# Kernel tuning notes

Measured on AMD Instinct MI355X. Metric: run time of the kernel, lower is better.

## Reference

```python
import math
import jax, jax.numpy as jnp
import numpy as np

D_MODEL = 1024
N_HEADS = 16
D_K = D_MODEL // N_HEADS
B, T = 2, 2048


def setup_inputs() -> dict:
    key = jax.random.key(0)
    kx, kq, kk, kv, ko = jax.random.split(key, 5)
    x = jax.random.normal(kx, (B, T, D_MODEL), dtype=jnp.float32)
    # causal mask, 1 = keep, 0 = masked (broadcast over batch & heads)
    mask = jnp.tril(jnp.ones((T, T), dtype=jnp.int32))[None, None, :, :]
    s = 1.0 / math.sqrt(D_MODEL)
    # nn.Linear stores weight as [out, in]; y = x @ W.T
    W_q = jax.random.normal(kq, (D_MODEL, D_MODEL), dtype=jnp.float32) * s
    W_k = jax.random.normal(kk, (D_MODEL, D_MODEL), dtype=jnp.float32) * s
    W_v = jax.random.normal(kv, (D_MODEL, D_MODEL), dtype=jnp.float32) * s
    W_o = jax.random.normal(ko, (D_MODEL, D_MODEL), dtype=jnp.float32) * s
    return {"x": x, "mask": mask, "W_q": W_q, "W_k": W_k, "W_v": W_v, "W_o": W_o}


def _split_heads(y):
    # [B,T,D] -> [B,H,T,d_k]
    b, t, _ = y.shape
    return y.reshape(b, t, N_HEADS, D_K).transpose(0, 2, 1, 3)


def reference(x, mask, W_q, W_k, W_v, W_o):
    Q = _split_heads(x @ W_q.T)
    K = _split_heads(x @ W_k.T)
    V = _split_heads(x @ W_v.T)
    scores = jnp.einsum("bhqd,bhkd->bhqk", Q, K) / math.sqrt(D_K)
    scores = jnp.where(mask == 0, -jnp.inf, scores)
    attn = jax.nn.softmax(scores, axis=-1)
    out = jnp.einsum("bhqk,bhkd->bhqd", attn, V)
    out = out.transpose(0, 2, 1, 3).reshape(x.shape[0], x.shape[1], D_MODEL)
    return out @ W_o.T
```

## Files before the change

### kernel.cpp

```cpp
#include <hip/hip_runtime.h>

typedef __attribute__((ext_vector_type(8))) short short8;
typedef __attribute__((ext_vector_type(4))) float f32x4;
typedef __attribute__((ext_vector_type(16))) float f32x16;
typedef __attribute__((ext_vector_type(4))) unsigned short u16x4;
typedef __attribute__((ext_vector_type(4))) unsigned int u32x4;

#define T_SEQ   2048
#define NHEADS  16
#define DHEAD   64
#define DMODEL  1024
#define NBATCH  2
#define MROWS   (NBATCH * T_SEQ)

__device__ __forceinline__ unsigned short f2bf(float f) {
    unsigned int u = __float_as_uint(f);
    u += 0x7fffu + ((u >> 16) & 1u);
    return (unsigned short)(u >> 16);
}

__device__ __forceinline__ unsigned int cvtpk(float lo, float hi) {
    unsigned int r;
    asm("v_cvt_pk_bf16_f32 %0, %1, %2" : "=v"(r) : "v"(lo), "v"(hi));
    return r;
}

__device__ __forceinline__ void pl32(int a, int b, int& r0, int& r1) {
    auto r = __builtin_amdgcn_permlane32_swap(a, b, false, false);
    r0 = r[0]; r1 = r[1];
}

__device__ __forceinline__ void gld_lds16(const void* g, void* l) {
    __builtin_amdgcn_global_load_lds(
        (const __attribute__((address_space(1))) void*)g,
        (__attribute__((address_space(3))) void*)l, 16, 0, 0);
}

#define N8X (MROWS * DMODEL / 8)
#define N8W (DMODEL * DMODEL / 8)
__global__ __launch_bounds__(256) void k_convert_all(const float* __restrict__ x,
                                                     const float* __restrict__ w0,
                                                     const float* __restrict__ w1,
                                                     const float* __restrict__ w2,
                                                     const float* __restrict__ w3,
                                                     unsigned short* __restrict__ xbf,
                                                     unsigned short* __restrict__ wbf) {
    int i = blockIdx.x * blockDim.x + threadIdx.x;
    const float* src;
    unsigned short* dst;
    if (i < N8X) {
        src = x + (size_t)i * 8;
        dst = xbf + (size_t)i * 8;
    } else {
        int j = i - N8X;
        int which = j >> 17;
        const float* w = (which == 0) ? w0 : (which == 1) ? w1 : (which == 2) ? w2 : w3;
        src = w + (size_t)(j & (N8W - 1)) * 8;
        dst = wbf + (size_t)j * 8;
    }
    const float4* p = (const float4*)src;
    float4 a = p[0], b = p[1];
    short8 r;
    r[0] = (short)f2bf(a.x); r[1] = (short)f2bf(a.y);
    r[2] = (short)f2bf(a.z); r[3] = (short)f2bf(a.w);
    r[4] = (short)f2bf(b.x); r[5] = (short)f2bf(b.y);
    r[6] = (short)f2bf(b.z); r[7] = (short)f2bf(b.w);
    *(short8*)dst = r;
}

template <int MODE>
__global__ __launch_bounds__(256) void k_gemm_st(const unsigned short* __restrict__ A,
                                                 const unsigned short* __restrict__ Wm,
                                                 float* __restrict__ outF,
                                                 unsigned short* __restrict__ outQ,
                                                 unsigned short* __restrict__ outK,
                                                 unsigned short* __restrict__ outV) {
    __shared__ __align__(16) unsigned short smA[2][128 * 32];
    __shared__ __align__(16) unsigned short smB[2][128 * 32];
    const int tid  = threadIdx.x;
    const int lane = tid & 63;
    const int w    = tid >> 6;
    const int lr   = lane & 15;
    const int lg   = lane >> 4;
    const int flat = blockIdx.x;
    const int x8   = flat & 7;
    const int jj_  = flat >> 3;
    const int n0   = (x8 + 8 * (jj_ >> 5)) * 128;
    const int m0   = (jj_ & 31) * 128;
    const int wm   = (w >> 1) * 64;
    const int wn   = (w & 1) * 64;

    const int srow = w * 32 + (lane >> 2);
    const int scol = (((lane & 3) ^ ((lane >> 3) & 3))) * 8;
    const unsigned short* gA0 = A  + (size_t)(m0 + srow) * DMODEL + scol;
    const unsigned short* gB0 = Wm + (size_t)(n0 + srow) * DMODEL + scol;
    const int lo = w * 1024;
    const int sw = (lg ^ ((lr >> 1) & 3)) * 8;

    f32x4 acc[4][4];
#pragma unroll
    for (int i = 0; i < 4; i++)
#pragma unroll
        for (int j = 0; j < 4; j++) acc[i][j] = (f32x4){0.f, 0.f, 0.f, 0.f};

#define STAGE(K0, BUF) do {                                            \
        gld_lds16(gA0 + (K0),               smA[BUF] + lo);            \
        gld_lds16(gA0 + 16 * DMODEL + (K0), smA[BUF] + lo + 16 * 32);  \
        gld_lds16(gB0 + (K0),               smB[BUF] + lo);            \
        gld_lds16(gB0 + 16 * DMODEL + (K0), smB[BUF] + lo + 16 * 32);  \
    } while (0)

#define FRAG_READ(BUF)                                                           \
        short8 af[4], bfr[4];                                                    \
        {                                                                        \
            const unsigned short* sA = smA[BUF];                                 \
            const unsigned short* sB = smB[BUF];                                 \
            _Pragma("unroll")                                                    \
            for (int i = 0; i < 4; i++)                                          \
                af[i] = *(const short8*)&sA[(wm + 16 * i + lr) * 32 + sw];       \
            _Pragma("unroll")                                                    \
            for (int j = 0; j < 4; j++)                                          \
                bfr[j] = *(const short8*)&sB[(wn + 16 * j + lr) * 32 + sw];      \
        }

#define MFMA16()                                                                 \
        _Pragma("unroll")                                                        \
        for (int i = 0; i < 4; i++)                                              \
            _Pragma("unroll")                                                    \
            for (int j = 0; j < 4; j++)                                          \
                acc[i][j] = __builtin_amdgcn_mfma_f32_16x16x32_bf16(             \
                    af[i], bfr[j], acc[i][j], 0, 0, 0);

    STAGE(0, 0);
    STAGE(32, 1);

    for (int t = 0; t < 30; ++t) {
        asm volatile("s_waitcnt vmcnt(4)" ::: "memory");
        __builtin_amdgcn_s_barrier();
        FRAG_READ(t & 1)
        asm volatile("s_waitcnt lgkmcnt(0)" ::: "memory");
        __builtin_amdgcn_sched_barrier(0);
        __builtin_amdgcn_s_barrier();
        STAGE((t + 2) * 32, t & 1);
        MFMA16()
    }
    {
        asm volatile("s_waitcnt vmcnt(4)" ::: "memory");
        __builtin_amdgcn_s_barrier();
        FRAG_READ(0)
        MFMA16()
    }
    {
        asm volatile("s_waitcnt vmcnt(0)" ::: "memory");
        __builtin_amdgcn_s_barrier();
        FRAG_READ(1)
        MFMA16()
    }
#undef STAGE
#undef FRAG_READ
#undef MFMA16

    if (MODE == 0) {
#pragma unroll
        for (int i = 0; i < 4; i++)
#pragma unroll
            for (int j = 0; j < 4; j++) {
                int n = n0 + wn + 16 * j + lr;
#pragma unroll
                for (int r = 0; r < 4; r++) {
                    int mm = m0 + wm + 16 * i + lg * 4 + r;
                    outF[(size_t)mm * DMODEL + n] = acc[i][j][r];
                }
            }
    } else {
        const int which = n0 >> 10;
        const int nb = n0 & 1023;
        const float QS = 0.18033688f;
#pragma unroll
        for (int i = 0; i < 4; i++)
#pragma unroll
            for (int j = 0; j < 4; j++) {
                int nloc = nb + wn + 16 * j + lr;
                int h = nloc >> 6, d = nloc & 63;
                int mb = m0 + wm + 16 * i + lg * 4;
                int b = mb >> 11, t = mb & (T_SEQ - 1);
                size_t base = (size_t)(b * NHEADS + h) * T_SEQ * DHEAD;
                if (which == 2) {
                    int off = ((((t >> 6) * 2 + (d >> 5)) * 4 + ((t >> 4) & 3)) * 64
                               + ((t >> 3) & 1) * 32 + (d & 31)) * 8 + (t & 7);
                    u16x4 pk;
#pragma unroll
                    for (int r = 0; r < 4; r++) pk[r] = f2bf(acc[i][j][r]);
                    *(u16x4*)(outV + base + off) = pk;
                } else {
                    unsigned short* dst = (which == 0) ? outQ : outK;
                    const float sc = (which == 0) ? QS : 1.0f;
                    int off = (((t >> 5) * 4 + (d >> 4)) * 64 + (d & 8) * 4 + (t & 31)) * 8 + (d & 7);
#pragma unroll
                    for (int r = 0; r < 4; r++)
                        dst[base + off + r * 8] = f2bf(acc[i][j][r] * sc);
                }
            }
    }
}

__global__ __launch_bounds__(256) void k_gemm_o(const unsigned short* __restrict__ A,
                                                const unsigned short* __restrict__ Wm,
                                                float* __restrict__ outF) {
    __shared__ __align__(16) unsigned short smA[2][64 * 32];
    __shared__ __align__(16) unsigned short smB[2][64 * 32];
    const int tid  = threadIdx.x;
    const int lane = tid & 63;
    const int w    = tid >> 6;
    const int lr   = lane & 15;
    const int lg   = lane >> 4;
    const int flat = blockIdx.x;
    const int x8   = flat & 7;
    const int jj_  = flat >> 3;
    const int n0   = (x8 + 8 * (jj_ >> 6)) * 64;
    const int m0   = (jj_ & 63) * 64;
    const int wm   = (w >> 1) * 32;
    const int wn   = (w & 1) * 32;

    const int sr   = w * 16 + (lane >> 2);
    const int scol = (((lane & 3) ^ ((lane >> 3) & 3))) * 8;
    const unsigned short* gA0 = A  + (size_t)(m0 + sr) * DMODEL + scol;
    const unsigned short* gB0 = Wm + (size_t)(n0 + sr) * DMODEL + scol;
    const int lo = w * 512;
    const int sw = (lg ^ ((lr >> 1) & 3)) * 8;

    f32x4 acc[2][2];
#pragma unroll
    for (int i = 0; i < 2; i++)
#pragma unroll
        for (int j = 0; j < 2; j++) acc[i][j] = (f32x4){0.f, 0.f, 0.f, 0.f};

#define STAGE(K0, BUF) do {                          \
        gld_lds16(gA0 + (K0), smA[BUF] + lo);        \
        gld_lds16(gB0 + (K0), smB[BUF] + lo);        \
    } while (0)

#define FRAG_READ(BUF)                                                           \
        short8 af[2], bfr[2];                                                    \
        {                                                                        \
            const unsigned short* sA = smA[BUF];                                 \
            const unsigned short* sB = smB[BUF];                                 \
            _Pragma("unroll")                                                    \
            for (int i = 0; i < 2; i++)                                          \
                af[i] = *(const short8*)&sA[(wm + 16 * i + lr) * 32 + sw];       \
            _Pragma("unroll")                                                    \
            for (int j = 0; j < 2; j++)                                          \
                bfr[j] = *(const short8*)&sB[(wn + 16 * j + lr) * 32 + sw];      \
        }

#define MFMA4()                                                                  \
        _Pragma("unroll")                                                        \
        for (int i = 0; i < 2; i++)                                              \
            _Pragma("unroll")                                                    \
            for (int j = 0; j < 2; j++)                                          \
                acc[i][j] = __builtin_amdgcn_mfma_f32_16x16x32_bf16(             \
                    af[i], bfr[j], acc[i][j], 0, 0, 0);

    STAGE(0, 0);
    STAGE(32, 1);

    for (int t = 0; t < 30; ++t) {
        asm volatile("s_waitcnt vmcnt(2)" ::: "memory");
        __builtin_amdgcn_s_barrier();
        FRAG_READ(t & 1)
        asm volatile("s_waitcnt lgkmcnt(0)" ::: "memory");
        __builtin_amdgcn_sched_barrier(0);
        __builtin_amdgcn_s_barrier();
        STAGE((t + 2) * 32, t & 1);
        MFMA4()
    }
    {
        asm volatile("s_waitcnt vmcnt(2)" ::: "memory");
        __builtin_amdgcn_s_barrier();
        FRAG_READ(0)
        MFMA4()
    }
    {
        asm volatile("s_waitcnt vmcnt(0)" ::: "memory");
        __builtin_amdgcn_s_barrier();
        FRAG_READ(1)
        MFMA4()
    }
#undef STAGE
#undef FRAG_READ
#undef MFMA4

#pragma unroll
    for (int i = 0; i < 2; i++)
#pragma unroll
        for (int j = 0; j < 2; j++) {
            int n = n0 + wn + 16 * j + lr;
#pragma unroll
            for (int r = 0; r < 4; r++) {
                int mm = m0 + wm + 16 * i + lg * 4 + r;
                outF[(size_t)mm * DMODEL + n] = acc[i][j][r];
            }
        }
}

__global__ __launch_bounds__(256) void k_attn(const unsigned short* __restrict__ Q,
                                              const unsigned short* __restrict__ K,
                                              const unsigned short* __restrict__ Vt,
                                              unsigned short* __restrict__ O) {
    __shared__ float Msm[3][64][33];
    const int tid  = threadIdx.x;
    const int lane = tid & 63;
    const int wv   = tid >> 6;
    const int l31  = lane & 31;
    const int hi   = lane >> 5;

    const int flat = blockIdx.x;
    const int xc   = flat & 7;
    const int rest = flat >> 3;
    const int hh   = rest >> 5;
    const int pr   = rest & 31;
    const int bh   = xc * 4 + hh;

    const size_t baseQK = (size_t)bh * T_SEQ * DHEAD;
    const unsigned short* Qb = Q  + baseQK;
    const unsigned short* Kb = K  + baseQK;
    const unsigned short* Vb = Vt + baseQK;

    for (int phase = 0; phase < 2; ++phase) {
        const int qt = phase ? pr : (63 - pr);
        const int q0 = qt * 32;
        const int ntiles = (qt >> 1) + 1;
        const int qlane = q0 + l31;

        short8 qf[4];
#pragma unroll
        for (int dt = 0; dt < 4; dt++)
            qf[dt] = *(const short8*)(Qb + ((size_t)(qt * 4 + dt) * 64 + lane) * 8);

        f32x16 oa0, oa1;
#pragma unroll
        for (int r = 0; r < 16; r++) { oa0[r] = 0.f; oa1[r] = 0.f; }
        float l = 0.f;

        const unsigned short* pK = Kb + (size_t)wv * 4096 + (size_t)lane * 8;
        const unsigned short* pV = Vb + (size_t)wv * 4096 + (size_t)lane * 8;

        for (int tix = wv; tix < ntiles; tix += 4) {
            f32x16 s0, s1;
#pragma unroll
            for (int r = 0; r < 16; r++) { s0[r] = 0.f; s1[r] = 0.f; }
            {
                short8 kf0[4], kf1[4];
#pragma unroll
                for (int kt = 0; kt < 4; kt++) {
                    kf0[kt] = *(const short8*)(pK + kt * 512);
                    kf1[kt] = *(const short8*)(pK + 2048 + kt * 512);
                }
                __builtin_amdgcn_s_setprio(1);
#pragma unroll
                for (int dt = 0; dt < 4; dt++)
                    s0 = __builtin_amdgcn_mfma_f32_32x32x16_bf16(kf0[dt], qf[dt], s0, 0, 0, 0);
#pragma unroll
                for (int dt = 0; dt < 4; dt++)
                    s1 = __builtin_amdgcn_mfma_f32_32x32x16_bf16(kf1[dt], qf[dt], s1, 0, 0, 0);
                __builtin_amdgcn_s_setprio(0);
            }

            short8 vf0[4], vf1[4];
#pragma unroll
            for (int kt = 0; kt < 4; kt++) {
                vf0[kt] = *(const short8*)(pV + kt * 512);
                vf1[kt] = *(const short8*)(pV + 2048 + kt * 512);
            }
            pK += 16384;
            pV += 16384;

            if (tix == ntiles - 1) {
                const int thr = qlane - tix * 64;
#pragma unroll
                for (int r = 0; r < 16; r++) {
                    const int koff = (r & 3) + 8 * (r >> 2) + 4 * hi;
                    if (koff > thr)      s0[r] = -1e30f;
                    if (koff + 32 > thr) s1[r] = -1e30f;
                }
            }

#pragma unroll
            for (int r = 0; r < 16; r++) {
                s0[r] = __builtin_amdgcn_exp2f(s0[r]);
                s1[r] = __builtin_amdgcn_exp2f(s1[r]);
            }
            float u8[8];
#pragma unroll
            for (int i = 0; i < 8; i++)
                u8[i] = (s0[i] + s0[i + 8]) + (s1[i] + s1[i + 8]);
            float u4a = u8[0] + u8[4], u4b = u8[1] + u8[5];
            float u4c = u8[2] + u8[6], u4d = u8[3] + u8[7];
            float sum = (u4a + u4b) + (u4c + u4d);
            {
                int r0, r1;
                pl32(__float_as_int(sum), __float_as_int(sum), r0, r1);
                sum = __int_as_float(r0) + __int_as_float(r1);
            }
            l += sum;

            unsigned int ow0[8], ow1[8];
#pragma unroll
            for (int q_ = 0; q_ < 8; q_++) {
                ow0[q_] = cvtpk(s0[2 * q_], s0[2 * q_ + 1]);
                ow1[q_] = cvtpk(s1[2 * q_], s1[2 * q_ + 1]);
            }

            __builtin_amdgcn_s_setprio(1);
#define PV_STEP(KT, OW, J) do {                                                  \
        int ra0, ra1, rb0, rb1;                                                  \
        pl32((int)OW[J],     (int)OW[J + 2], ra0, ra1);                          \
        pl32((int)OW[J + 1], (int)OW[J + 3], rb0, rb1);                          \
        u32x4 wvv;                                                               \
        wvv[0] = (unsigned)ra0; wvv[1] = (unsigned)rb0;                          \
        wvv[2] = (unsigned)ra1; wvv[3] = (unsigned)rb1;                          \
        short8 pf = __builtin_bit_cast(short8, wvv);                             \
        oa0 = __builtin_amdgcn_mfma_f32_32x32x16_bf16(vf0[KT], pf, oa0, 0, 0, 0);\
        oa1 = __builtin_amdgcn_mfma_f32_32x32x16_bf16(vf1[KT], pf, oa1, 0, 0, 0);\
    } while (0)

            PV_STEP(0, ow0, 0);
            PV_STEP(1, ow0, 4);
            PV_STEP(2, ow1, 0);
            PV_STEP(3, ow1, 4);
#undef PV_STEP
            __builtin_amdgcn_s_setprio(0);
        }

        const int merger = phase;
        if (phase == 1) __syncthreads();
        if (wv != merger) {
            const int slot = wv - (wv > merger ? 1 : 0);
#pragma unroll
            for (int r = 0; r < 16; r++) {
                Msm[slot][lane][r]      = oa0[r];
                Msm[slot][lane][16 + r] = oa1[r];
            }
            Msm[slot][lane][32] = l;
        }
        __syncthreads();
        if (wv == merger) {
            float lt = l;
#pragma unroll
            for (int s = 0; s < 3; s++) lt += Msm[s][lane][32];
            const float inv = 1.0f / lt;
            const int b = bh >> 4, h = bh & 15;
            unsigned short* orow = O + ((size_t)(b * T_SEQ + qlane)) * DMODEL + h * DHEAD;
#pragma unroll
            for (int rg = 0; rg < 4; rg++) {
                u16x4 pk0, pk1;
#pragma unroll
                for (int jj = 0; jj < 4; jj++) {
                    const int idx = 4 * rg + jj;
                    float v0 = oa0[idx];
                    float v1 = oa1[idx];
#pragma unroll
                    for (int s = 0; s < 3; s++) {
                        v0 += Msm[s][lane][idx];
                        v1 += Msm[s][lane][16 + idx];
                    }
                    pk0[jj] = f2bf(v0 * inv);
                    pk1[jj] = f2bf(v1 * inv);
                }
                *(u16x4*)(orow + 4 * hi + 8 * rg) = pk0;
                *(u16x4*)(orow + 32 + 4 * hi + 8 * rg) = pk1;
            }
        }
    }
}

extern "C" void kernel_launch(void* const* d_in, const int* in_sizes, int n_in,
                              void* d_out, int out_size, void* d_ws, size_t ws_size,
                              hipStream_t stream) {
    const float* x  = (const float*)d_in[0];
    const float* Wq = (const float*)d_in[2];
    const float* Wk = (const float*)d_in[3];
    const float* Wv = (const float*)d_in[4];
    const float* Wo = (const float*)d_in[5];

    unsigned short* wsu = (unsigned short*)d_ws;
    const size_t WELE = (size_t)DMODEL * DMODEL;
    unsigned short* Wo_bf = wsu + 3 * WELE;
    unsigned short* x_bf  = wsu + 4 * WELE;
    unsigned short* Qp    = wsu + 8 * WELE;
    unsigned short* Kp    = wsu + 12 * WELE;
    unsigned short* Vp    = wsu + 16 * WELE;
    if (ws_size < 20 * WELE * sizeof(unsigned short)) return;

    const int nAll = N8X + 4 * N8W;
    k_convert_all<<<dim3(nAll / 256), 256, 0, stream>>>(x, Wq, Wk, Wv, Wo, x_bf, wsu);

    k_gemm_st<1><<<dim3(768), 256, 0, stream>>>(
        x_bf, wsu, nullptr, Qp, Kp, Vp);

    k_attn<<<dim3(1024), 256, 0, stream>>>(Qp, Kp, Vp, x_bf);

    k_gemm_o<<<dim3(1024), 256, 0, stream>>>(
        x_bf, Wo_bf, (float*)d_out);
}
```

Measured before the change: 99.06 us.

## Share double-buffered K/V tiles in LDS across four query-tile waves

The attention kernel changes its work split. Each block now handles four consecutive 32-row query tiles, one per wave, and all four waves walk the full key range together. Before, the four waves split the key tiles of a single query tile and merged partial results through shared memory. K/V tiles are now loaded once per block into a double-buffered LDS area with direct global-to-LDS loads and then reused by all waves, which removes the cross-wave merge and halves the grid. In exchange it adds two barriers per tile, and waves with shorter causal extents sit idle while the longest wave in the block finishes.

```diff
diff --git a/kernel.cpp b/kernel.cpp
--- a/kernel.cpp
+++ b/kernel.cpp
@@ -307,7 +307,7 @@
                                               const unsigned short* __restrict__ K,
                                               const unsigned short* __restrict__ Vt,
                                               unsigned short* __restrict__ O) {
-    __shared__ float Msm[3][64][33];
+    __shared__ __align__(16) unsigned short KV[2][8192];
     const int tid  = threadIdx.x;
     const int lane = tid & 63;
     const int wv   = tid >> 6;
@@ -317,8 +317,8 @@
     const int flat = blockIdx.x;
     const int xc   = flat & 7;
     const int rest = flat >> 3;
-    const int hh   = rest >> 5;
-    const int pr   = rest & 31;
+    const int hh   = rest >> 4;
+    const int kq   = rest & 15;
     const int bh   = xc * 4 + hh;
 
     const size_t baseQK = (size_t)bh * T_SEQ * DHEAD;
@@ -326,11 +326,23 @@
     const unsigned short* Kb = K  + baseQK;
     const unsigned short* Vb = Vt + baseQK;
 
+    const int ldsc = wv * 1024;
+
+#define AST(TT, B) do {                                                          \
+        const unsigned short* ks_ = Kb + (size_t)(TT) * 4096 + ldsc + lane * 8;  \
+        const unsigned short* vs_ = Vb + (size_t)(TT) * 4096 + ldsc + lane * 8;  \
+        gld_lds16(ks_,       &KV[B][ldsc]);                                      \
+        gld_lds16(ks_ + 512, &KV[B][ldsc + 512]);                                \
+        gld_lds16(vs_,       &KV[B][4096 + ldsc]);                               \
+        gld_lds16(vs_ + 512, &KV[B][4096 + ldsc + 512]);                         \
+    } while (0)
+
     for (int phase = 0; phase < 2; ++phase) {
-        const int qt = phase ? pr : (63 - pr);
-        const int q0 = qt * 32;
-        const int ntiles = (qt >> 1) + 1;
-        const int qlane = q0 + l31;
+        const int qb = phase ? (4 * kq) : (60 - 4 * kq);
+        const int qt = qb + wv;
+        const int qlane = qt * 32 + l31;
+        const int own_ext = (qt >> 1) + 1;
+        const int ext_max = ((qb + 3) >> 1) + 1;
 
         short8 qf[4];
 #pragma unroll
@@ -342,20 +354,27 @@
         for (int r = 0; r < 16; r++) { oa0[r] = 0.f; oa1[r] = 0.f; }
         float l = 0.f;
 
-        const unsigned short* pK = Kb + (size_t)wv * 4096 + (size_t)lane * 8;
-        const unsigned short* pV = Vb + (size_t)wv * 4096 + (size_t)lane * 8;
-
-        for (int tix = wv; tix < ntiles; tix += 4) {
+        AST(0, 0);
+        AST(1, 1);
+
+        for (int t = 0; t < ext_max; ++t) {
+            asm volatile("s_waitcnt vmcnt(4)" ::: "memory");
+            __builtin_amdgcn_s_barrier();
+            const bool act = (t < own_ext);
+            const unsigned short* kb_ = &KV[t & 1][lane * 8];
+
             f32x16 s0, s1;
 #pragma unroll
             for (int r = 0; r < 16; r++) { s0[r] = 0.f; s1[r] = 0.f; }
-            {
+            if (act) {
                 short8 kf0[4], kf1[4];
 #pragma unroll
                 for (int kt = 0; kt < 4; kt++) {
-                    kf0[kt] = *(const short8*)(pK + kt * 512);
-                    kf1[kt] = *(const short8*)(pK + 2048 + kt * 512);
-                }
+                    kf0[kt] = *(const short8*)(kb_ + kt * 512);
+                    kf1[kt] = *(const short8*)(kb_ + 2048 + kt * 512);
+                }
+                asm volatile("s_waitcnt lgkmcnt(0)" ::: "memory");
+                __builtin_amdgcn_sched_barrier(0);
                 __builtin_amdgcn_s_setprio(1);
 #pragma unroll
                 for (int dt = 0; dt < 4; dt++)
@@ -365,53 +384,53 @@
                     s1 = __builtin_amdgcn_mfma_f32_32x32x16_bf16(kf1[dt], qf[dt], s1, 0, 0, 0);
                 __builtin_amdgcn_s_setprio(0);
             }
-
             short8 vf0[4], vf1[4];
-#pragma unroll
-            for (int kt = 0; kt < 4; kt++) {
-                vf0[kt] = *(const short8*)(pV + kt * 512);
-                vf1[kt] = *(const short8*)(pV + 2048 + kt * 512);
-            }
-            pK += 16384;
-            pV += 16384;
-
-            if (tix == ntiles - 1) {
-                const int thr = qlane - tix * 64;
+            if (act) {
+#pragma unroll
+                for (int kt = 0; kt < 4; kt++) {
+                    vf0[kt] = *(const short8*)(kb_ + 4096 + kt * 512);
+                    vf1[kt] = *(const short8*)(kb_ + 6144 + kt * 512);
+                }
+            }
+            asm volatile("s_waitcnt lgkmcnt(0)" ::: "memory");
+            __builtin_amdgcn_sched_barrier(0);
+            __builtin_amdgcn_s_barrier();
+            {
+                int tn = t + 2;
+                if (tn > ext_max - 1) tn = ext_max - 1;
+                AST(tn, t & 1);
+            }
+
+            if (act) {
+                if (t == own_ext - 1) {
+                    const int thr = qlane - t * 64;
+#pragma unroll
+                    for (int r = 0; r < 16; r++) {
+                        const int koff = (r & 3) + 8 * (r >> 2) + 4 * hi;
+                        if (koff > thr)      s0[r] = -1e30f;
+                        if (koff + 32 > thr) s1[r] = -1e30f;
+                    }
+                }
 #pragma unroll
                 for (int r = 0; r < 16; r++) {
-                    const int koff = (r & 3) + 8 * (r >> 2) + 4 * hi;
-                    if (koff > thr)      s0[r] = -1e30f;
-                    if (koff + 32 > thr) s1[r] = -1e30f;
-                }
-            }
-
-#pragma unroll
-            for (int r = 0; r < 16; r++) {
-                s0[r] = __builtin_amdgcn_exp2f(s0[r]);
-                s1[r] = __builtin_amdgcn_exp2f(s1[r]);
-            }
-            float u8[8];
-#pragma unroll
-            for (int i = 0; i < 8; i++)
-                u8[i] = (s0[i] + s0[i + 8]) + (s1[i] + s1[i + 8]);
-            float u4a = u8[0] + u8[4], u4b = u8[1] + u8[5];
-            float u4c = u8[2] + u8[6], u4d = u8[3] + u8[7];
-            float sum = (u4a + u4b) + (u4c + u4d);
-            {
-                int r0, r1;
-                pl32(__float_as_int(sum), __float_as_int(sum), r0, r1);
-                sum = __int_as_float(r0) + __int_as_float(r1);
-            }
-            l += sum;
-
-            unsigned int ow0[8], ow1[8];
-#pragma unroll
-            for (int q_ = 0; q_ < 8; q_++) {
-                ow0[q_] = cvtpk(s0[2 * q_], s0[2 * q_ + 1]);
-                ow1[q_] = cvtpk(s1[2 * q_], s1[2 * q_ + 1]);
-            }
-
-            __builtin_amdgcn_s_setprio(1);
+                    s0[r] = __builtin_amdgcn_exp2f(s0[r]);
+                    s1[r] = __builtin_amdgcn_exp2f(s1[r]);
+                }
+                float u8[8];
+#pragma unroll
+                for (int i = 0; i < 8; i++)
+                    u8[i] = (s0[i] + s0[i + 8]) + (s1[i] + s1[i + 8]);
+                float u4a = u8[0] + u8[4], u4b = u8[1] + u8[5];
+                float u4c = u8[2] + u8[6], u4d = u8[3] + u8[7];
+                l += (u4a + u4b) + (u4c + u4d);
+
+                unsigned int ow0[8], ow1[8];
+#pragma unroll
+                for (int q_ = 0; q_ < 8; q_++) {
+                    ow0[q_] = cvtpk(s0[2 * q_], s0[2 * q_ + 1]);
+                    ow1[q_] = cvtpk(s1[2 * q_], s1[2 * q_ + 1]);
+                }
+                __builtin_amdgcn_s_setprio(1);
 #define PV_STEP(KT, OW, J) do {                                                  \
         int ra0, ra1, rb0, rb1;                                                  \
         pl32((int)OW[J],     (int)OW[J + 2], ra0, ra1);                          \
@@ -423,31 +442,22 @@
         oa0 = __builtin_amdgcn_mfma_f32_32x32x16_bf16(vf0[KT], pf, oa0, 0, 0, 0);\
         oa1 = __builtin_amdgcn_mfma_f32_32x32x16_bf16(vf1[KT], pf, oa1, 0, 0, 0);\
     } while (0)
-
-            PV_STEP(0, ow0, 0);
-            PV_STEP(1, ow0, 4);
-            PV_STEP(2, ow1, 0);
-            PV_STEP(3, ow1, 4);
+                PV_STEP(0, ow0, 0);
+                PV_STEP(1, ow0, 4);
+                PV_STEP(2, ow1, 0);
+                PV_STEP(3, ow1, 4);
 #undef PV_STEP
-            __builtin_amdgcn_s_setprio(0);
+                __builtin_amdgcn_s_setprio(0);
+            }
         }
 
-        const int merger = phase;
-        if (phase == 1) __syncthreads();
-        if (wv != merger) {
-            const int slot = wv - (wv > merger ? 1 : 0);
-#pragma unroll
-            for (int r = 0; r < 16; r++) {
-                Msm[slot][lane][r]      = oa0[r];
-                Msm[slot][lane][16 + r] = oa1[r];
-            }
-            Msm[slot][lane][32] = l;
-        }
-        __syncthreads();
-        if (wv == merger) {
-            float lt = l;
-#pragma unroll
-            for (int s = 0; s < 3; s++) lt += Msm[s][lane][32];
+        asm volatile("s_waitcnt vmcnt(0)" ::: "memory");
+        __builtin_amdgcn_s_barrier();
+
+        {
+            int r0, r1;
+            pl32(__float_as_int(l), __float_as_int(l), r0, r1);
+            const float lt = __int_as_float(r0) + __int_as_float(r1);
             const float inv = 1.0f / lt;
             const int b = bh >> 4, h = bh & 15;
             unsigned short* orow = O + ((size_t)(b * T_SEQ + qlane)) * DMODEL + h * DHEAD;
@@ -457,21 +467,15 @@
 #pragma unroll
                 for (int jj = 0; jj < 4; jj++) {
                     const int idx = 4 * rg + jj;
-                    float v0 = oa0[idx];
-                    float v1 = oa1[idx];
-#pragma unroll
-                    for (int s = 0; s < 3; s++) {
-                        v0 += Msm[s][lane][idx];
-                        v1 += Msm[s][lane][16 + idx];
-                    }
-                    pk0[jj] = f2bf(v0 * inv);
-                    pk1[jj] = f2bf(v1 * inv);
+                    pk0[jj] = f2bf(oa0[idx] * inv);
+                    pk1[jj] = f2bf(oa1[idx] * inv);
                 }
                 *(u16x4*)(orow + 4 * hi + 8 * rg) = pk0;
                 *(u16x4*)(orow + 32 + 4 * hi + 8 * rg) = pk1;
             }
         }
     }
+#undef AST
 }
 
 extern "C" void kernel_launch(void* const* d_in, const int* in_sizes, int n_in,
@@ -498,7 +502,7 @@
     k_gemm_st<1><<<dim3(768), 256, 0, stream>>>(
         x_bf, wsu, nullptr, Qp, Kp, Vp);
 
-    k_attn<<<dim3(1024), 256, 0, stream>>>(Qp, Kp, Vp, x_bf);
+    k_attn<<<dim3(512), 256, 0, stream>>>(Qp, Kp, Vp, x_bf);
 
     k_gemm_o<<<dim3(1024), 256, 0, stream>>>(
         x_bf, Wo_bf, (float*)d_out);
```

Result: slower. 115.1 us (+16.2%).
